# Kernel optimization log

Measured on AMD Instinct MI355X. Metric: run time of the kernel, lower is better.

The kernel has to match this reference:

```python
import jax, jax.numpy as jnp
import numpy as np
from jax import lax

N_TOKENS = 524288
N_EXPERTS = 64
TOP_K = 8


def setup_inputs() -> dict:
    key = jax.random.key(0)
    logits = jax.random.normal(key, (N_TOKENS, N_EXPERTS), dtype=jnp.float32)
    # expert_counts / assignments / offsets are output buffers in the torch
    # module (filled by the custom kernel); pass zero placeholders.
    return {
        "expert_counts": jnp.zeros((N_EXPERTS,), dtype=jnp.int32),
        "assignments": jnp.zeros((N_TOKENS, TOP_K), dtype=jnp.int32),
        "offsets": jnp.zeros((N_TOKENS, TOP_K), dtype=jnp.int32),
        "logits": logits,
    }


def reference(expert_counts, assignments, offsets, logits):
    """Ragged top-k gating (replay_routing=False).

    Returns (expert_counts, scores, assignments, offsets, logits_out):
      scores       [N, K]  top-k softmax probabilities per token
      assignments  [N, K]  top-k expert ids per token
      offsets      [N, K]  slot of each (token, k) within its expert's
                           ragged bucket (token-major arrival order)
      expert_counts[E]     number of routed slots per expert
      logits_out           pass-through copy of logits
    """
    N, E = logits.shape
    K = assignments.shape[1]

    probs = jax.nn.softmax(logits, axis=-1)            # [N, E]
    scores, assign = lax.top_k(probs, K)               # [N, K] each
    assign = assign.astype(jnp.int32)

    flat = assign.reshape(-1)                          # [N*K], token-major
    counts = jnp.zeros((E,), jnp.int32).at[flat].add(1)

    # offsets: rank of each slot among equal-expert slots in arrival order.
    # Stable sort by expert id; within-expert rank = sorted position minus
    # the expert's segment start (exclusive cumsum of counts).
    order = jnp.argsort(flat, stable=True)             # [N*K]
    sorted_e = flat[order]
    starts = jnp.concatenate(
        [jnp.zeros((1,), jnp.int32), jnp.cumsum(counts)[:-1].astype(jnp.int32)]
    )                                                  # [E]
    ranks = jnp.arange(N * K, dtype=jnp.int32) - starts[sorted_e]
    offs = jnp.zeros((N * K,), jnp.int32).at[order].set(ranks).reshape(N, K)

    return counts, scores, assign, offs, logits
```

## Files before the change

### kernel.cpp

```cpp
#include <hip/hip_runtime.h>

#define NT 524288
#define NE 64
#define NK 8
#define TPB 128
#define NBLK (NT / TPB)
#define SPB (TPB * NK)

__global__ __launch_bounds__(256) void topk_kernel(
    const float* __restrict__ logits,
    float* __restrict__ out_scores,
    float* __restrict__ out_assign,
    float* __restrict__ out_packed,
    float* __restrict__ out_logits,
    int* __restrict__ blockCounts)
{
    __shared__ int assign_lds[SPB];
    __shared__ int running[NE];
    __shared__ int wcnt[4][NE];

    const int t = threadIdx.x;
    const int b = blockIdx.x;
    const int g = t & 7;
    const int tok_in_pass = t >> 3;

    for (int pass = 0; pass < 4; ++pass) {
        const int ltok = pass * 32 + tok_in_pass;
        const int token = b * TPB + ltok;
        const float* lp = logits + (size_t)token * NE + g * 8;
        float4 v0 = *(const float4*)lp;
        float4 v1 = *(const float4*)(lp + 4);
        float* op = out_logits + (size_t)token * NE + g * 8;
        *(float4*)op = v0;
        *(float4*)(op + 4) = v1;

        float l[8] = {v0.x, v0.y, v0.z, v0.w, v1.x, v1.y, v1.z, v1.w};

        float m = l[0];
        #pragma unroll
        for (int j = 1; j < 8; ++j) m = fmaxf(m, l[j]);
        #pragma unroll
        for (int sh = 1; sh < 8; sh <<= 1) m = fmaxf(m, __shfl_xor(m, sh, 64));

        float p[8];
        float s = 0.f;
        #pragma unroll
        for (int j = 0; j < 8; ++j) { p[j] = expf(l[j] - m); s += p[j]; }
        #pragma unroll
        for (int sh = 1; sh < 8; sh <<= 1) s += __shfl_xor(s, sh, 64);
        #pragma unroll
        for (int j = 0; j < 8; ++j) p[j] = p[j] / s;

        float sc = 0.f; int id = 0;
        #pragma unroll
        for (int k = 0; k < NK; ++k) {
            float bv = p[0]; int bi = 0;
            #pragma unroll
            for (int j = 1; j < 8; ++j)
                if (p[j] > bv) { bv = p[j]; bi = j; }
            int bidx = g * 8 + bi;
            #pragma unroll
            for (int sh = 1; sh < 8; sh <<= 1) {
                float ov = __shfl_xor(bv, sh, 64);
                int   oi = __shfl_xor(bidx, sh, 64);
                if (ov > bv || (ov == bv && oi < bidx)) { bv = ov; bidx = oi; }
            }
            if (g == k) { sc = bv; id = bidx; }
            #pragma unroll
            for (int j = 0; j < 8; ++j)
                p[j] = (bidx == g * 8 + j) ? -1.0f : p[j];
        }

        const size_t slot = (size_t)token * NK + g;
        out_scores[slot] = sc;
        out_assign[slot] = (float)id;
        assign_lds[ltok * NK + g] = id;
    }

    if (t < NE) running[t] = 0;
    __syncthreads();

    const int w = t >> 6;
    const int l = t & 63;
    const unsigned long long lt_mask = (l == 0) ? 0ull : ((~0ull) >> (64 - l));

    for (int tile = 0; tile < 4; ++tile) {
        const int slot_l = tile * 256 + t;
        const int e = assign_lds[slot_l];

        unsigned long long mask = ~0ull;
        #pragma unroll
        for (int bit = 0; bit < 6; ++bit) {
            unsigned long long bb = __ballot((e >> bit) & 1);
            mask &= ((e >> bit) & 1) ? bb : ~bb;
        }
        const int r_in_wave = __popcll(mask & lt_mask);
        const int wc = __popcll(mask);

        wcnt[w][l] = 0;
        __syncthreads();
        if ((mask & lt_mask) == 0ull) wcnt[w][e] = wc;
        __syncthreads();

        int before = running[e];
        for (int w2 = 0; w2 < w; ++w2) before += wcnt[w2][e];
        const int rank = before + r_in_wave;

        const int gslot = b * SPB + slot_l;
        out_packed[gslot] = (float)(rank * 64 + e);

        __syncthreads();
        if (t < NE) running[t] += wcnt[0][t] + wcnt[1][t] + wcnt[2][t] + wcnt[3][t];
        __syncthreads();
    }

    if (t < NE) blockCounts[b * NE + t] = running[t];
}

__global__ __launch_bounds__(256) void scan_kernel(
    int* __restrict__ blockCounts, float* __restrict__ out_counts)
{
    __shared__ int sdata[256];
    const int e = blockIdx.x;
    const int t = threadIdx.x;
    const int PER = NBLK / 256;

    int s = 0;
    for (int i = 0; i < PER; ++i) s += blockCounts[(t * PER + i) * NE + e];
    sdata[t] = s;
    __syncthreads();

    for (int off = 1; off < 256; off <<= 1) {
        int v = (t >= off) ? sdata[t - off] : 0;
        __syncthreads();
        sdata[t] += v;
        __syncthreads();
    }
    int run = (t == 0) ? 0 : sdata[t - 1];

    for (int i = 0; i < PER; ++i) {
        const int idx = (t * PER + i) * NE + e;
        const int c = blockCounts[idx];
        blockCounts[idx] = run;
        run += c;
    }
    if (t == 255) out_counts[e] = (float)sdata[255];
}

__global__ __launch_bounds__(256) void offs_kernel(
    const int* __restrict__ blockCounts, float* __restrict__ out_packed)
{
    __shared__ int base[NE];
    const int b = blockIdx.x;
    const int t = threadIdx.x;
    if (t < NE) base[t] = blockCounts[b * NE + t];
    __syncthreads();
    #pragma unroll
    for (int tile = 0; tile < 4; ++tile) {
        const int gslot = b * SPB + tile * 256 + t;
        const int packed = (int)out_packed[gslot];
        const int e = packed & 63;
        const int rank = packed >> 6;
        out_packed[gslot] = (float)(base[e] + rank);
    }
}

extern "C" void kernel_launch(void* const* d_in, const int* in_sizes, int n_in,
                              void* d_out, int out_size, void* d_ws, size_t ws_size,
                              hipStream_t stream) {
    const float* logits = (const float*)d_in[3];

    float* out = (float*)d_out;
    float* out_counts = out;
    float* out_scores = out + NE;
    float* out_assign = out_scores + (size_t)NT * NK;
    float* out_offs   = out_assign + (size_t)NT * NK;
    float* out_logits = out_offs + (size_t)NT * NK;

    int* blockCounts = (int*)d_ws;

    hipLaunchKernelGGL(topk_kernel, dim3(NBLK), dim3(256), 0, stream,
                       logits, out_scores, out_assign, out_offs, out_logits,
                       blockCounts);
    hipLaunchKernelGGL(scan_kernel, dim3(NE), dim3(256), 0, stream,
                       blockCounts, out_counts);
    hipLaunchKernelGGL(offs_kernel, dim3(NBLK), dim3(256), 0, stream,
                       blockCounts, out_offs);
}
```

Baseline: 334.3 us.

## Compute softmax and top-k with one thread per token instead of eight

Each token is now handled by a single thread that holds all 64 logits in registers. It computes softmax and an 8-round top-k serially, with no cross-lane shuffles. Each block now covers 256 tokens, and expert ids are packed into one 64-bit LDS word per token for the ranking phase. The aim is to remove shuffle-heavy reductions and redundant per-lane work. In exchange it raises register pressure, lowers occupancy, and gives uncoalesced strided global loads and stores per thread.

```diff
diff --git a/kernel.cpp b/kernel.cpp
--- a/kernel.cpp
+++ b/kernel.cpp
@@ -3,9 +3,10 @@
 #define NT 524288
 #define NE 64
 #define NK 8
-#define TPB 128
+#define TPB 256
 #define NBLK (NT / TPB)
 #define SPB (TPB * NK)
+#define NTILE (SPB / 256)
 
 __global__ __launch_bounds__(256) void topk_kernel(
     const float* __restrict__ logits,
@@ -15,67 +16,72 @@
     float* __restrict__ out_logits,
     int* __restrict__ blockCounts)
 {
-    __shared__ int assign_lds[SPB];
+    __shared__ unsigned long long pack_lds[TPB];
     __shared__ int running[NE];
     __shared__ int wcnt[4][NE];
 
     const int t = threadIdx.x;
     const int b = blockIdx.x;
-    const int g = t & 7;
-    const int tok_in_pass = t >> 3;
+    const int token = b * TPB + t;
 
-    for (int pass = 0; pass < 4; ++pass) {
-        const int ltok = pass * 32 + tok_in_pass;
-        const int token = b * TPB + ltok;
-        const float* lp = logits + (size_t)token * NE + g * 8;
-        float4 v0 = *(const float4*)lp;
-        float4 v1 = *(const float4*)(lp + 4);
-        float* op = out_logits + (size_t)token * NE + g * 8;
-        *(float4*)op = v0;
-        *(float4*)(op + 4) = v1;
+    const float* lp = logits + (size_t)token * NE;
+    float* op = out_logits + (size_t)token * NE;
 
-        float l[8] = {v0.x, v0.y, v0.z, v0.w, v1.x, v1.y, v1.z, v1.w};
+    float p[64];
+    float m = -__builtin_inff();
+    #pragma unroll
+    for (int i = 0; i < 16; ++i) {
+        float4 v = ((const float4*)lp)[i];
+        ((float4*)op)[i] = v;
+        p[4*i+0] = v.x; p[4*i+1] = v.y; p[4*i+2] = v.z; p[4*i+3] = v.w;
+        m = fmaxf(m, fmaxf(fmaxf(v.x, v.y), fmaxf(v.z, v.w)));
+    }
 
-        float m = l[0];
+    #pragma unroll
+    for (int j = 0; j < 64; ++j) p[j] = expf(p[j] - m);
+
+    float s8[8];
+    #pragma unroll
+    for (int g = 0; g < 8; ++g) {
+        float ss = p[g*8];
         #pragma unroll
-        for (int j = 1; j < 8; ++j) m = fmaxf(m, l[j]);
+        for (int j = 1; j < 8; ++j) ss += p[g*8 + j];
+        s8[g] = ss;
+    }
+    float t1[8], t2[8];
+    #pragma unroll
+    for (int g = 0; g < 8; ++g) t1[g] = s8[g] + s8[g ^ 1];
+    #pragma unroll
+    for (int g = 0; g < 8; ++g) t2[g] = t1[g] + t1[g ^ 2];
+    const float s = t2[0] + t2[4];
+
+    #pragma unroll
+    for (int j = 0; j < 64; ++j) p[j] = p[j] / s;
+
+    float sc[8]; int id[8];
+    #pragma unroll
+    for (int k = 0; k < NK; ++k) {
+        float bv = p[0]; int bi = 0;
         #pragma unroll
-        for (int sh = 1; sh < 8; sh <<= 1) m = fmaxf(m, __shfl_xor(m, sh, 64));
+        for (int j = 1; j < 64; ++j)
+            if (p[j] > bv) { bv = p[j]; bi = j; }
+        sc[k] = bv; id[k] = bi;
+        #pragma unroll
+        for (int j = 0; j < 64; ++j)
+            p[j] = (bi == j) ? -1.0f : p[j];
+    }
 
-        float p[8];
-        float s = 0.f;
-        #pragma unroll
-        for (int j = 0; j < 8; ++j) { p[j] = expf(l[j] - m); s += p[j]; }
-        #pragma unroll
-        for (int sh = 1; sh < 8; sh <<= 1) s += __shfl_xor(s, sh, 64);
-        #pragma unroll
-        for (int j = 0; j < 8; ++j) p[j] = p[j] / s;
+    float* sp = out_scores + (size_t)token * NK;
+    ((float4*)sp)[0] = make_float4(sc[0], sc[1], sc[2], sc[3]);
+    ((float4*)sp)[1] = make_float4(sc[4], sc[5], sc[6], sc[7]);
+    float* ap = out_assign + (size_t)token * NK;
+    ((float4*)ap)[0] = make_float4((float)id[0], (float)id[1], (float)id[2], (float)id[3]);
+    ((float4*)ap)[1] = make_float4((float)id[4], (float)id[5], (float)id[6], (float)id[7]);
 
-        float sc = 0.f; int id = 0;
-        #pragma unroll
-        for (int k = 0; k < NK; ++k) {
-            float bv = p[0]; int bi = 0;
-            #pragma unroll
-            for (int j = 1; j < 8; ++j)
-                if (p[j] > bv) { bv = p[j]; bi = j; }
-            int bidx = g * 8 + bi;
-            #pragma unroll
-            for (int sh = 1; sh < 8; sh <<= 1) {
-                float ov = __shfl_xor(bv, sh, 64);
-                int   oi = __shfl_xor(bidx, sh, 64);
-                if (ov > bv || (ov == bv && oi < bidx)) { bv = ov; bidx = oi; }
-            }
-            if (g == k) { sc = bv; id = bidx; }
-            #pragma unroll
-            for (int j = 0; j < 8; ++j)
-                p[j] = (bidx == g * 8 + j) ? -1.0f : p[j];
-        }
-
-        const size_t slot = (size_t)token * NK + g;
-        out_scores[slot] = sc;
-        out_assign[slot] = (float)id;
-        assign_lds[ltok * NK + g] = id;
-    }
+    unsigned long long pk = 0;
+    #pragma unroll
+    for (int k = 0; k < NK; ++k) pk |= (unsigned long long)id[k] << (6 * k);
+    pack_lds[t] = pk;
 
     if (t < NE) running[t] = 0;
     __syncthreads();
@@ -84,9 +90,9 @@
     const int l = t & 63;
     const unsigned long long lt_mask = (l == 0) ? 0ull : ((~0ull) >> (64 - l));
 
-    for (int tile = 0; tile < 4; ++tile) {
+    for (int tile = 0; tile < NTILE; ++tile) {
         const int slot_l = tile * 256 + t;
-        const int e = assign_lds[slot_l];
+        const int e = (int)((pack_lds[slot_l >> 3] >> ((slot_l & 7) * 6)) & 63);
 
         unsigned long long mask = ~0ull;
         #pragma unroll
@@ -106,8 +112,7 @@
         for (int w2 = 0; w2 < w; ++w2) before += wcnt[w2][e];
         const int rank = before + r_in_wave;
 
-        const int gslot = b * SPB + slot_l;
-        out_packed[gslot] = (float)(rank * 64 + e);
+        out_packed[(size_t)b * SPB + slot_l] = (float)(rank * 64 + e);
 
         __syncthreads();
         if (t < NE) running[t] += wcnt[0][t] + wcnt[1][t] + wcnt[2][t] + wcnt[3][t];
@@ -156,12 +161,10 @@
     if (t < NE) base[t] = blockCounts[b * NE + t];
     __syncthreads();
     #pragma unroll
-    for (int tile = 0; tile < 4; ++tile) {
-        const int gslot = b * SPB + tile * 256 + t;
+    for (int tile = 0; tile < NTILE; ++tile) {
+        const size_t gslot = (size_t)b * SPB + tile * 256 + t;
         const int packed = (int)out_packed[gslot];
-        const int e = packed & 63;
-        const int rank = packed >> 6;
-        out_packed[gslot] = (float)(base[e] + rank);
+        out_packed[gslot] = (float)(base[packed & 63] + (packed >> 6));
     }
 }
 
```

Measured after the change: 381.0 us. 14.0% more time.
